# Kernel tuning notes

Hardware: AMD Instinct MI355X
Metric: run time of the kernel (lower is better)

The kernel has to match this reference:

```python
import jax, jax.numpy as jnp
import numpy as np

B, T, D = 32, 4096, 96        # batch, frames, codebook_dim
N_CB, K = 6, 384              # n_codebooks, codebook_size
PROJ, W2V = 192, 768          # semantic_proj_dim, w2v_bert_dim
COMMIT = 0.5


def setup_inputs() -> dict:
    key = jax.random.key(0)
    ks = jax.random.split(key, 7)
    z = jax.random.normal(ks[0], (B, T, D), jnp.float32)
    w2v_targets = jax.random.normal(ks[1], (B, T, W2V), jnp.float32)
    # torch init: uniform(-1/K, 1/K) per codebook
    codebooks = jax.random.uniform(ks[2], (N_CB, K, D), jnp.float32, -1.0 / K, 1.0 / K)
    w1 = jax.random.normal(ks[3], (D, PROJ), jnp.float32) * 0.02
    b1 = jnp.zeros((PROJ,), jnp.float32)
    w2 = jax.random.normal(ks[4], (PROJ, W2V), jnp.float32) * 0.02
    b2 = jnp.zeros((W2V,), jnp.float32)
    return {"z": z, "w2v_targets": w2v_targets, "codebooks": codebooks,
            "w1": w1, "b1": b1, "w2": w2, "b2": b2}


def _quantize(residual, emb):
    """One VQ stage: squared-L2 nearest code + gather. residual: (B,T,D), emb: (K,D)."""
    flat = residual.reshape(-1, D)                                   # (BT, D)
    dist = (jnp.sum(flat * flat, axis=1, keepdims=True)
            - 2.0 * flat @ emb.T
            + jnp.sum(emb * emb, axis=1))                            # (BT, K)
    idx = jnp.argmin(dist, axis=1).reshape(B, T)                     # (B, T)
    z_q = emb[idx]                                                   # (B, T, D) gather
    return z_q, idx


def reference(z, w2v_targets, codebooks, w1, b1, w2, b2):
    sg = jax.lax.stop_gradient
    residual = z
    z_q_total = jnp.zeros_like(z)
    codes = []
    vq_loss = jnp.float32(0.0)
    semantic_loss = jnp.float32(0.0)
    for i in range(N_CB):
        z_q, idx = _quantize(residual, codebooks[i])
        commitment_loss = jnp.mean((sg(z_q) - residual) ** 2)
        embedding_loss = jnp.mean((z_q - sg(residual)) ** 2)
        vq_loss = vq_loss + embedding_loss + COMMIT * commitment_loss
        z_q_st = residual + sg(z_q - residual)                       # straight-through
        if i == 0:
            h = jax.nn.gelu(z_q_st @ w1 + b1, approximate=False)
            pred = h @ w2 + b2                                       # (B, T, W2V)
            semantic_loss = jnp.mean((pred - w2v_targets) ** 2)
        z_q_total = z_q_total + z_q_st
        residual = residual - sg(z_q_st)
        codes.append(idx)
    all_codes = jnp.stack(codes, axis=-1)                            # (B, T, N_CB)
    return z_q_total, all_codes, vq_loss, semantic_loss
```

## Files before the change

### kernel.cpp

```cpp
#include <hip/hip_runtime.h>
#include <hip/hip_bf16.h>

#define BT    131072
#define DD    96
#define KCB   384
#define NCB   6
#define PROJ  192
#define W2V   768

#define ZQT_OFF   0L
#define CODES_OFF 12582912L
#define VQ_OFF    13369344L
#define SEM_OFF   13369345L

#define ACC_OFF   0L
#define E32_OFF   64L
#define W1T_OFF   9280L
#define W2T_OFF   46144L

typedef __attribute__((ext_vector_type(8))) short  bf16x8;
typedef __attribute__((ext_vector_type(4))) float  f32x4;

static __device__ __forceinline__ unsigned short f2bf(float x) {
    __hip_bfloat16 h = __float2bfloat16(x);
    return *reinterpret_cast<unsigned short*>(&h);
}
static __device__ __forceinline__ float comp(const float4& v, int c) {
    return c == 0 ? v.x : c == 1 ? v.y : c == 2 ? v.z : v.w;
}

static __device__ __forceinline__ float pairwise96_sq(const float4* r) {
    float a[8];
#pragma unroll
    for (int j = 0; j < 8; ++j) {
        const int c = j & 3, base = j >> 2;
        float x0 = comp(r[base], c);
        float s  = __fmul_rn(x0, x0);
#pragma unroll
        for (int t = 1; t < 12; ++t) {
            float x = comp(r[base + 2 * t], c);
            s = __fadd_rn(s, __fmul_rn(x, x));
        }
        a[j] = s;
    }
    return __fadd_rn(__fadd_rn(__fadd_rn(a[0], a[1]), __fadd_rn(a[2], a[3])),
                     __fadd_rn(__fadd_rn(a[4], a[5]), __fadd_rn(a[6], a[7])));
}

__global__ void kzero(double* __restrict__ acc) {
    if (threadIdx.x < 8) acc[threadIdx.x] = 0.0;
}

__global__ void kee(const float* __restrict__ cb, float* __restrict__ E32) {
    int c = blockIdx.x * 256 + threadIdx.x;
    if (c < NCB * KCB) {
        const float* row = cb + (size_t)c * DD;
        float a[8];
#pragma unroll
        for (int j = 0; j < 8; ++j) a[j] = __fmul_rn(row[j], row[j]);
        for (int t = 1; t < 12; ++t) {
#pragma unroll
            for (int j = 0; j < 8; ++j) {
                float x = row[8 * t + j];
                a[j] = __fadd_rn(a[j], __fmul_rn(x, x));
            }
        }
        E32[c] = __fadd_rn(__fadd_rn(__fadd_rn(a[0], a[1]), __fadd_rn(a[2], a[3])),
                           __fadd_rn(__fadd_rn(a[4], a[5]), __fadd_rn(a[6], a[7])));
    }
}

__global__ void kwt(const float* __restrict__ w1, const float* __restrict__ w2,
                    __hip_bfloat16* __restrict__ w1T, __hip_bfloat16* __restrict__ w2T) {
    int i = blockIdx.x * 256 + threadIdx.x;
    if (i < DD * PROJ) {
        int n = i / DD, k = i % DD;
        w1T[i] = __float2bfloat16(w1[k * PROJ + n]);
    }
    int j = i - DD * PROJ;
    if (j >= 0 && j < PROJ * W2V) {
        int n = j / PROJ, k = j % PROJ;
        w2T[j] = __float2bfloat16(w2[k * W2V + n]);
    }
}

__global__ __launch_bounds__(128, 2) void kq(
        const float* __restrict__ z, const float* __restrict__ cb,
        const float* __restrict__ E32, float* __restrict__ dout) {
    __shared__ float et2[64 * DD];
    const int  tid  = threadIdx.x;
    const long tok0 = (long)blockIdx.x * 256 + tid;
    const long tok1 = tok0 + 128;

    float4 r0[24], r1[24];
    const float4* z4a = (const float4*)(z + tok0 * DD);
    const float4* z4b = (const float4*)(z + tok1 * DD);
#pragma unroll
    for (int i = 0; i < 24; ++i) { r0[i] = z4a[i]; r1[i] = z4b[i]; }

    for (int s = 0; s < NCB; ++s) {
        const float S0 = pairwise96_sq(r0);
        const float S1 = pairwise96_sq(r1);
        float m0v = 3.4e38f, m1v = 3.4e38f;
        int   b0 = 0, b1 = 0;
        for (int c = 0; c < 6; ++c) {
            __syncthreads();
            const float4* src = (const float4*)(cb + (size_t)(s * KCB + c * 64) * DD);
            float4* dst = (float4*)et2;
#pragma unroll
            for (int j = 0; j < 12; ++j) {
                float4 v = src[j * 128 + tid];
                v.x = __fmul_rn(2.f, v.x); v.y = __fmul_rn(2.f, v.y);
                v.z = __fmul_rn(2.f, v.z); v.w = __fmul_rn(2.f, v.w);
                dst[j * 128 + tid] = v;
            }
            __syncthreads();
            const float* eec = E32 + s * KCB + c * 64;
#pragma unroll 2
            for (int kl = 0; kl < 64; ++kl) {
                const float4* e4p = ((const float4*)et2) + kl * 24;
                float a0 = 0.f, a1 = 0.f;
#pragma unroll
                for (int i = 0; i < 24; ++i) {
                    float4 e = e4p[i];
                    a0 = fmaf(r0[i].x, e.x, a0); a0 = fmaf(r0[i].y, e.y, a0);
                    a0 = fmaf(r0[i].z, e.z, a0); a0 = fmaf(r0[i].w, e.w, a0);
                    a1 = fmaf(r1[i].x, e.x, a1); a1 = fmaf(r1[i].y, e.y, a1);
                    a1 = fmaf(r1[i].z, e.z, a1); a1 = fmaf(r1[i].w, e.w, a1);
                }
                float d0 = __fadd_rn(__fsub_rn(S0, a0), eec[kl]);
                float d1 = __fadd_rn(__fsub_rn(S1, a1), eec[kl]);
                const int kk = c * 64 + kl;
                if (d0 < m0v) { m0v = d0; b0 = kk; }
                if (d1 < m1v) { m1v = d1; b1 = kk; }
            }
        }
        dout[CODES_OFF + tok0 * NCB + s] = (float)b0;
        dout[CODES_OFF + tok1 * NCB + s] = (float)b1;
        const float4* q04 = (const float4*)(cb + ((size_t)s * KCB + b0) * DD);
        const float4* q14 = (const float4*)(cb + ((size_t)s * KCB + b1) * DD);
#pragma unroll
        for (int i = 0; i < 24; ++i) {
            float4 qa = q04[i], qb = q14[i];
            float4 da, sa, db, sb;
            da.x = __fsub_rn(qa.x, r0[i].x); da.y = __fsub_rn(qa.y, r0[i].y);
            da.z = __fsub_rn(qa.z, r0[i].z); da.w = __fsub_rn(qa.w, r0[i].w);
            sa.x = __fadd_rn(r0[i].x, da.x); sa.y = __fadd_rn(r0[i].y, da.y);
            sa.z = __fadd_rn(r0[i].z, da.z); sa.w = __fadd_rn(r0[i].w, da.w);
            r0[i].x = __fsub_rn(r0[i].x, sa.x); r0[i].y = __fsub_rn(r0[i].y, sa.y);
            r0[i].z = __fsub_rn(r0[i].z, sa.z); r0[i].w = __fsub_rn(r0[i].w, sa.w);
            db.x = __fsub_rn(qb.x, r1[i].x); db.y = __fsub_rn(qb.y, r1[i].y);
            db.z = __fsub_rn(qb.z, r1[i].z); db.w = __fsub_rn(qb.w, r1[i].w);
            sb.x = __fadd_rn(r1[i].x, db.x); sb.y = __fadd_rn(r1[i].y, db.y);
            sb.z = __fadd_rn(r1[i].z, db.z); sb.w = __fadd_rn(r1[i].w, db.w);
            r1[i].x = __fsub_rn(r1[i].x, sb.x); r1[i].y = __fsub_rn(r1[i].y, sb.y);
            r1[i].z = __fsub_rn(r1[i].z, sb.z); r1[i].w = __fsub_rn(r1[i].w, sb.w);
        }
    }
}

__global__ __launch_bounds__(256) void kr(
        const float* __restrict__ z, const float* __restrict__ cb,
        const float* __restrict__ codesf, float* __restrict__ zqt_out,
        double* __restrict__ acc) {
    const long tok = (long)blockIdx.x * 256 + threadIdx.x;
    float4 r[24], zqt[24];
    const float4* z4 = (const float4*)(z + tok * DD);
#pragma unroll
    for (int i = 0; i < 24; ++i) r[i] = z4[i];
    double ls[NCB];
#pragma unroll
    for (int s = 0; s < NCB; ++s) {
        const int idx = (int)codesf[tok * NCB + s];
        const float4* q4 = (const float4*)(cb + (size_t)(s * KCB + idx) * DD);
        double a = 0.0;
#pragma unroll
        for (int i = 0; i < 24; ++i) {
            float4 q = q4[i];
            float4 d, st;
            d.x = __fsub_rn(q.x, r[i].x); d.y = __fsub_rn(q.y, r[i].y);
            d.z = __fsub_rn(q.z, r[i].z); d.w = __fsub_rn(q.w, r[i].w);
            st.x = __fadd_rn(r[i].x, d.x); st.y = __fadd_rn(r[i].y, d.y);
            st.z = __fadd_rn(r[i].z, d.z); st.w = __fadd_rn(r[i].w, d.w);
            if (s == 0) {
                zqt[i] = st;
            } else {
                zqt[i].x = __fadd_rn(zqt[i].x, st.x); zqt[i].y = __fadd_rn(zqt[i].y, st.y);
                zqt[i].z = __fadd_rn(zqt[i].z, st.z); zqt[i].w = __fadd_rn(zqt[i].w, st.w);
            }
            r[i].x = __fsub_rn(r[i].x, st.x); r[i].y = __fsub_rn(r[i].y, st.y);
            r[i].z = __fsub_rn(r[i].z, st.z); r[i].w = __fsub_rn(r[i].w, st.w);
            a += (double)d.x * (double)d.x; a += (double)d.y * (double)d.y;
            a += (double)d.z * (double)d.z; a += (double)d.w * (double)d.w;
        }
        ls[s] = a;
    }
    float4* o4 = (float4*)(zqt_out + tok * DD);
#pragma unroll
    for (int i = 0; i < 24; ++i) o4[i] = zqt[i];
#pragma unroll
    for (int s = 0; s < NCB; ++s) {
        double v = ls[s];
        for (int off = 32; off > 0; off >>= 1) v += __shfl_down(v, off, 64);
        if ((threadIdx.x & 63) == 0) atomicAdd(&acc[s], v);
    }
}

__global__ __launch_bounds__(256) void kh(
        const float* __restrict__ z, const float* __restrict__ cb,
        const float* __restrict__ codesf,
        const __hip_bfloat16* __restrict__ w1T, const float* __restrict__ b1,
        const __hip_bfloat16* __restrict__ w2T, const float* __restrict__ b2,
        const float* __restrict__ tgt, double* __restrict__ sem_acc) {
    __shared__ unsigned short hs[64][PROJ + 8];
    const int lane = threadIdx.x & 63, wv = threadIdx.x >> 6;
    const int col  = lane & 15, quad = lane >> 4;
    const long m0  = (long)blockIdx.x * 64 + wv * 16;

    const long tokrow = m0 + col;
    const int  code0  = (int)codesf[tokrow * NCB];
    const float* zr = z  + tokrow * DD;
    const float* qr = cb + (size_t)code0 * DD;
    bf16x8 a1f[3];
#pragma unroll
    for (int ks = 0; ks < 3; ++ks) {
        const int k0 = ks * 32 + quad * 8;
        bf16x8 v;
#pragma unroll
        for (int j = 0; j < 8; ++j) {
            float r = zr[k0 + j], q = qr[k0 + j];
            float d  = __fsub_rn(q, r);
            float st = __fadd_rn(r, d);
            v[j] = (short)f2bf(st);
        }
        a1f[ks] = v;
    }
    for (int nt = 0; nt < 12; ++nt) {
        const int n0 = nt * 16;
        f32x4 accv = {0.f, 0.f, 0.f, 0.f};
        const unsigned short* bw = (const unsigned short*)w1T + (n0 + col) * DD + quad * 8;
#pragma unroll
        for (int ks = 0; ks < 3; ++ks) {
            bf16x8 bf = *(const bf16x8*)(bw + ks * 32);
            accv = __builtin_amdgcn_mfma_f32_16x16x32_bf16(a1f[ks], bf, accv, 0, 0, 0);
        }
#pragma unroll
        for (int r = 0; r < 4; ++r) {
            float x = accv[r] + b1[n0 + col];
            float g = 0.5f * x * (1.0f + erff(x * 0.70710678118654752440f));
            hs[wv * 16 + quad * 4 + r][n0 + col] = f2bf(g);
        }
    }
    __syncthreads();
    bf16x8 a2f[6];
#pragma unroll
    for (int ks = 0; ks < 6; ++ks)
        a2f[ks] = *(const bf16x8*)(&hs[wv * 16 + col][ks * 32 + quad * 8]);
    double lsum = 0.0;
    for (int nt = 0; nt < 48; ++nt) {
        const int n0 = nt * 16;
        f32x4 accv = {0.f, 0.f, 0.f, 0.f};
        const unsigned short* bw = (const unsigned short*)w2T + (size_t)(n0 + col) * PROJ + quad * 8;
#pragma unroll
        for (int ks = 0; ks < 6; ++ks) {
            bf16x8 bf = *(const bf16x8*)(bw + ks * 32);
            accv = __builtin_amdgcn_mfma_f32_16x16x32_bf16(a2f[ks], bf, accv, 0, 0, 0);
        }
#pragma unroll
        for (int r = 0; r < 4; ++r) {
            float pred = accv[r] + b2[n0 + col];
            float dt = pred - tgt[(m0 + quad * 4 + r) * (long)W2V + n0 + col];
            lsum += (double)dt * (double)dt;
        }
    }
    for (int off = 32; off > 0; off >>= 1) lsum += __shfl_down(lsum, off, 64);
    if (lane == 0) atomicAdd(sem_acc, lsum);
}

__global__ void kf(const double* __restrict__ acc, float* __restrict__ dout) {
    if (threadIdx.x == 0 && blockIdx.x == 0) {
        float vq = 0.f;
        for (int s = 0; s < NCB; ++s) {
            float l = (float)(acc[s] / 12582912.0);
            vq = vq + l;
            vq = vq + 0.5f * l;
        }
        dout[VQ_OFF]  = vq;
        dout[SEM_OFF] = (float)(acc[6] / 100663296.0);
    }
}

extern "C" void kernel_launch(void* const* d_in, const int* in_sizes, int n_in,
                              void* d_out, int out_size, void* d_ws, size_t ws_size,
                              hipStream_t stream) {
    const float* z   = (const float*)d_in[0];
    const float* tgt = (const float*)d_in[1];
    const float* cb  = (const float*)d_in[2];
    const float* w1  = (const float*)d_in[3];
    const float* b1  = (const float*)d_in[4];
    const float* w2  = (const float*)d_in[5];
    const float* b2  = (const float*)d_in[6];
    float* out = (float*)d_out;
    char*  ws  = (char*)d_ws;

    double*          accs = (double*)(ws + ACC_OFF);
    float*           E32  = (float*)(ws + E32_OFF);
    __hip_bfloat16*  w1T  = (__hip_bfloat16*)(ws + W1T_OFF);
    __hip_bfloat16*  w2T  = (__hip_bfloat16*)(ws + W2T_OFF);

    kzero<<<dim3(1), dim3(64), 0, stream>>>(accs);
    kee  <<<dim3(9), dim3(256), 0, stream>>>(cb, E32);
    kwt  <<<dim3(648), dim3(256), 0, stream>>>(w1, w2, w1T, w2T);
    kq   <<<dim3(512), dim3(128), 0, stream>>>(z, cb, E32, out);
    kr   <<<dim3(512), dim3(256), 0, stream>>>(z, cb, out + CODES_OFF, out, accs);
    kh   <<<dim3(2048), dim3(256), 0, stream>>>(z, cb, out + CODES_OFF,
                                                w1T, b1, w2T, b2, tgt, accs + 6);
    kf   <<<dim3(1), dim3(64), 0, stream>>>(accs, out);
}
```

Before: 2.354 ms.

## Register-tile VQ distance search across tokens and codes, split codebook across waves

```diff
diff --git a/kernel.cpp b/kernel.cpp
--- a/kernel.cpp
+++ b/kernel.cpp
@@ -18,6 +18,10 @@
 #define W1T_OFF   9280L
 #define W2T_OFF   46144L
 
+#define TT 4
+#define CT 24
+#define TB 256
+
 typedef __attribute__((ext_vector_type(8))) short  bf16x8;
 typedef __attribute__((ext_vector_type(4))) float  f32x4;
 
@@ -84,78 +88,129 @@
     }
 }
 
-__global__ __launch_bounds__(128, 2) void kq(
+__global__ __launch_bounds__(256, 2) void kq2(
         const float* __restrict__ z, const float* __restrict__ cb,
-        const float* __restrict__ E32, float* __restrict__ dout) {
-    __shared__ float et2[64 * DD];
-    const int  tid  = threadIdx.x;
-    const long tok0 = (long)blockIdx.x * 256 + tid;
-    const long tok1 = tok0 + 128;
-
-    float4 r0[24], r1[24];
-    const float4* z4a = (const float4*)(z + tok0 * DD);
-    const float4* z4b = (const float4*)(z + tok1 * DD);
-#pragma unroll
-    for (int i = 0; i < 24; ++i) { r0[i] = z4a[i]; r1[i] = z4b[i]; }
-
+        const float* __restrict__ E32, float* __restrict__ dout,
+        float4* __restrict__ rg) {
+    __shared__ __align__(16) float  e_lds[4][CT * DD];
+    __shared__ __align__(16) float2 comb[4][TB];
+    __shared__ __align__(16) float  S_lds[TB];
+
+    const int tid = threadIdx.x, lane = tid & 63, w = tid >> 6;
+    const long tok0 = (long)blockIdx.x * TB;
+
+    {
+        const long t = tok0 + tid;
+        const float4* z4 = (const float4*)(z + t * DD);
+        float4 r[24];
+#pragma unroll
+        for (int i = 0; i < 24; ++i) r[i] = z4[i];
+        S_lds[tid] = pairwise96_sq(r);
+#pragma unroll
+        for (int i = 0; i < 24; ++i) rg[(long)i * BT + t] = r[i];
+    }
+    __syncthreads();
+
+#pragma unroll 1
     for (int s = 0; s < NCB; ++s) {
-        const float S0 = pairwise96_sq(r0);
-        const float S1 = pairwise96_sq(r1);
-        float m0v = 3.4e38f, m1v = 3.4e38f;
-        int   b0 = 0, b1 = 0;
-        for (int c = 0; c < 6; ++c) {
-            __syncthreads();
-            const float4* src = (const float4*)(cb + (size_t)(s * KCB + c * 64) * DD);
-            float4* dst = (float4*)et2;
-#pragma unroll
-            for (int j = 0; j < 12; ++j) {
-                float4 v = src[j * 128 + tid];
-                v.x = __fmul_rn(2.f, v.x); v.y = __fmul_rn(2.f, v.y);
-                v.z = __fmul_rn(2.f, v.z); v.w = __fmul_rn(2.f, v.w);
-                dst[j * 128 + tid] = v;
-            }
-            __syncthreads();
-            const float* eec = E32 + s * KCB + c * 64;
-#pragma unroll 2
-            for (int kl = 0; kl < 64; ++kl) {
-                const float4* e4p = ((const float4*)et2) + kl * 24;
-                float a0 = 0.f, a1 = 0.f;
+        float Sj[TT];
+#pragma unroll
+        for (int j = 0; j < TT; ++j) Sj[j] = S_lds[64 * j + lane];
+        float mv[TT]; int bi[TT];
+#pragma unroll
+        for (int j = 0; j < TT; ++j) { mv[j] = 3.4e38f; bi[j] = 0; }
+
+#pragma unroll 1
+        for (int ct = 0; ct < 96 / CT; ++ct) {
+            const int cbase = w * 96 + ct * CT;
+            {
+                const float4* esrc = (const float4*)(cb + ((size_t)s * KCB + cbase) * DD);
+                float4* edst = (float4*)&e_lds[w][0];
+#pragma unroll
+                for (int i = 0; i < 9; ++i) edst[i * 64 + lane] = esrc[i * 64 + lane];
+            }
+            float acc[CT][TT];
+#pragma unroll
+            for (int c = 0; c < CT; ++c)
+#pragma unroll
+                for (int j = 0; j < TT; ++j) acc[c][j] = 0.f;
+
+            float4 rv[TT];
+#pragma unroll
+            for (int j = 0; j < TT; ++j) rv[j] = rg[tok0 + 64 * j + lane];
+#pragma unroll 1
+            for (int kt = 0; kt < 24; ++kt) {
+                float4 rnx[TT];
+                if (kt < 23) {
+#pragma unroll
+                    for (int j = 0; j < TT; ++j)
+                        rnx[j] = rg[(long)(kt + 1) * BT + tok0 + 64 * j + lane];
+                }
+                float4 r2[TT];
+#pragma unroll
+                for (int j = 0; j < TT; ++j) {
+                    r2[j].x = __fmul_rn(2.f, rv[j].x); r2[j].y = __fmul_rn(2.f, rv[j].y);
+                    r2[j].z = __fmul_rn(2.f, rv[j].z); r2[j].w = __fmul_rn(2.f, rv[j].w);
+                }
+                const float* eb = &e_lds[w][kt * 4];
+#pragma unroll
+                for (int c = 0; c < CT; ++c) {
+                    float4 e = *(const float4*)(eb + c * DD);
+#pragma unroll
+                    for (int j = 0; j < TT; ++j) {
+                        acc[c][j] = fmaf(r2[j].x, e.x, acc[c][j]);
+                        acc[c][j] = fmaf(r2[j].y, e.y, acc[c][j]);
+                        acc[c][j] = fmaf(r2[j].z, e.z, acc[c][j]);
+                        acc[c][j] = fmaf(r2[j].w, e.w, acc[c][j]);
+                    }
+                }
+#pragma unroll
+                for (int j = 0; j < TT; ++j) rv[j] = rnx[j];
+            }
+#pragma unroll
+            for (int c = 0; c < CT; ++c) {
+                const float E = E32[s * KCB + cbase + c];
+#pragma unroll
+                for (int j = 0; j < TT; ++j) {
+                    float d = __fadd_rn(__fsub_rn(Sj[j], acc[c][j]), E);
+                    if (d < mv[j]) { mv[j] = d; bi[j] = cbase + c; }
+                }
+            }
+        }
+#pragma unroll
+        for (int j = 0; j < TT; ++j)
+            comb[w][64 * j + lane] = make_float2(mv[j], (float)bi[j]);
+        __syncthreads();
+
+        {
+            const long t = tok0 + tid;
+            float bv = comb[0][tid].x; int bidx = (int)comb[0][tid].y;
+#pragma unroll
+            for (int w2 = 1; w2 < 4; ++w2) {
+                float2 cnd = comb[w2][tid];
+                if (cnd.x < bv) { bv = cnd.x; bidx = (int)cnd.y; }
+            }
+            dout[CODES_OFF + t * NCB + s] = (float)bidx;
+            if (s < NCB - 1) {
+                const float4* q4 = (const float4*)(cb + ((size_t)s * KCB + bidx) * DD);
+                float4 rn[24];
 #pragma unroll
                 for (int i = 0; i < 24; ++i) {
-                    float4 e = e4p[i];
-                    a0 = fmaf(r0[i].x, e.x, a0); a0 = fmaf(r0[i].y, e.y, a0);
-                    a0 = fmaf(r0[i].z, e.z, a0); a0 = fmaf(r0[i].w, e.w, a0);
-                    a1 = fmaf(r1[i].x, e.x, a1); a1 = fmaf(r1[i].y, e.y, a1);
-                    a1 = fmaf(r1[i].z, e.z, a1); a1 = fmaf(r1[i].w, e.w, a1);
-                }
-                float d0 = __fadd_rn(__fsub_rn(S0, a0), eec[kl]);
-                float d1 = __fadd_rn(__fsub_rn(S1, a1), eec[kl]);
-                const int kk = c * 64 + kl;
-                if (d0 < m0v) { m0v = d0; b0 = kk; }
-                if (d1 < m1v) { m1v = d1; b1 = kk; }
-            }
-        }
-        dout[CODES_OFF + tok0 * NCB + s] = (float)b0;
-        dout[CODES_OFF + tok1 * NCB + s] = (float)b1;
-        const float4* q04 = (const float4*)(cb + ((size_t)s * KCB + b0) * DD);
-        const float4* q14 = (const float4*)(cb + ((size_t)s * KCB + b1) * DD);
-#pragma unroll
-        for (int i = 0; i < 24; ++i) {
-            float4 qa = q04[i], qb = q14[i];
-            float4 da, sa, db, sb;
-            da.x = __fsub_rn(qa.x, r0[i].x); da.y = __fsub_rn(qa.y, r0[i].y);
-            da.z = __fsub_rn(qa.z, r0[i].z); da.w = __fsub_rn(qa.w, r0[i].w);
-            sa.x = __fadd_rn(r0[i].x, da.x); sa.y = __fadd_rn(r0[i].y, da.y);
-            sa.z = __fadd_rn(r0[i].z, da.z); sa.w = __fadd_rn(r0[i].w, da.w);
-            r0[i].x = __fsub_rn(r0[i].x, sa.x); r0[i].y = __fsub_rn(r0[i].y, sa.y);
-            r0[i].z = __fsub_rn(r0[i].z, sa.z); r0[i].w = __fsub_rn(r0[i].w, sa.w);
-            db.x = __fsub_rn(qb.x, r1[i].x); db.y = __fsub_rn(qb.y, r1[i].y);
-            db.z = __fsub_rn(qb.z, r1[i].z); db.w = __fsub_rn(qb.w, r1[i].w);
-            sb.x = __fadd_rn(r1[i].x, db.x); sb.y = __fadd_rn(r1[i].y, db.y);
-            sb.z = __fadd_rn(r1[i].z, db.z); sb.w = __fadd_rn(r1[i].w, db.w);
-            r1[i].x = __fsub_rn(r1[i].x, sb.x); r1[i].y = __fsub_rn(r1[i].y, sb.y);
-            r1[i].z = __fsub_rn(r1[i].z, sb.z); r1[i].w = __fsub_rn(r1[i].w, sb.w);
-        }
+                    float4 rv = rg[(long)i * BT + t], q = q4[i];
+                    float4 d, st;
+                    d.x = __fsub_rn(q.x, rv.x); d.y = __fsub_rn(q.y, rv.y);
+                    d.z = __fsub_rn(q.z, rv.z); d.w = __fsub_rn(q.w, rv.w);
+                    st.x = __fadd_rn(rv.x, d.x); st.y = __fadd_rn(rv.y, d.y);
+                    st.z = __fadd_rn(rv.z, d.z); st.w = __fadd_rn(rv.w, d.w);
+                    rn[i].x = __fsub_rn(rv.x, st.x); rn[i].y = __fsub_rn(rv.y, st.y);
+                    rn[i].z = __fsub_rn(rv.z, st.z); rn[i].w = __fsub_rn(rv.w, st.w);
+                }
+                S_lds[tid] = pairwise96_sq(rn);
+#pragma unroll
+                for (int i = 0; i < 24; ++i) rg[(long)i * BT + t] = rn[i];
+            }
+        }
+        __syncthreads();
     }
 }
 
@@ -311,7 +366,8 @@
     kzero<<<dim3(1), dim3(64), 0, stream>>>(accs);
     kee  <<<dim3(9), dim3(256), 0, stream>>>(cb, E32);
     kwt  <<<dim3(648), dim3(256), 0, stream>>>(w1, w2, w1T, w2T);
-    kq   <<<dim3(512), dim3(128), 0, stream>>>(z, cb, E32, out);
+    kq2  <<<dim3(BT / TB), dim3(256), 0, stream>>>(z, cb, E32, out,
+                                                   (float4*)(out + ZQT_OFF));
     kr   <<<dim3(512), dim3(256), 0, stream>>>(z, cb, out + CODES_OFF, out, accs);
     kh   <<<dim3(2048), dim3(256), 0, stream>>>(z, cb, out + CODES_OFF,
                                                 w1T, b1, w2T, b2, tgt, accs + 6);
```

Measured after the change: 1.896 ms. 19.5% less time.
